# Performance work log

Hardware: AMD Instinct MI355X
Metric: run time of the kernel (lower is better)

## Reference

```python
import jax, jax.numpy as jnp
import numpy as np


def _lyndon_indices(c, d):
    """All Lyndon words of length <= d over alphabet {0..c-1} via Duval's algorithm,
    mapped to flat indices into the flattened signature (levels 1..d concatenated,
    first letter most significant within each level). Static numpy computation."""
    words = []
    w = [-1]
    while w:
        w[-1] += 1
        words.append(tuple(w))
        m = len(w)
        while len(w) < d:
            w.append(w[len(w) - m])
        while w and w[-1] == c - 1:
            w.pop()
    words.sort(key=lambda t: (len(t), t))  # group by word length, lexicographic within
    offsets = np.concatenate([[0], np.cumsum([c ** k for k in range(1, d + 1)])])
    idx = []
    for word in words:
        pos = 0
        for letter in word:
            pos = pos * c + letter
        idx.append(int(offsets[len(word) - 1]) + pos)
    return np.asarray(idx, dtype=np.int64)


def _split_levels(sig, c, d):
    levels, start = [], 0
    for k in range(1, d + 1):
        n = c ** k
        levels.append(sig[:, start:start + n])  # (B, c^k)
        start += n
    return levels


def _mul_by_S(P, S, d):
    """Graded product P (x) S in the truncated tensor algebra (zero scalar parts).
    P[i], S[i] are level-(i+1) components of shape (B, c^(i+1)) or None."""
    B = S[0].shape[0]
    out = [None] * d
    for m in range(d):  # output level m+1
        acc = None
        for i in range(m):  # P level i+1 combines with S level m-i
            if P[i] is None:
                continue
            t = jnp.einsum('bi,bj->bij', P[i], S[m - 1 - i]).reshape(B, -1)
            acc = t if acc is None else acc + t
        out[m] = acc
    return out


def _log_signature_flat(sig, c, d):
    """log(1 + S) truncated at depth d, flattened levels 1..d."""
    S = _split_levels(sig, c, d)
    L = list(S)  # n=1 term (coefficient +1)
    P = S
    for n in range(2, d + 1):
        P = _mul_by_S(P, S, d)  # P = S^{(x) n}, levels < n are None
        coef = ((-1.0) ** (n + 1)) / n
        for k in range(d):
            if P[k] is not None:
                L[k] = L[k] + coef * P[k]
    return jnp.concatenate(L, axis=1)


def setup_inputs() -> dict:
    key = jax.random.key(0)
    channels, depth, batch = 8, 6, 64
    width = sum(channels ** k for k in range(1, depth + 1))  # 299592
    signature = jax.random.normal(key, (batch, width), dtype=jnp.float32) * 0.1
    return {"signature": signature, "channels": channels, "depth": depth}


def reference(signature, channels, depth):
    idx = jnp.asarray(_lyndon_indices(channels, depth))
    log_sig = _log_signature_flat(signature, channels, depth)  # (B, width)
    return log_sig[:, idx]  # Lyndon-word coefficients ('words' mode)
```

## Files before the change

### kernel.cpp

```cpp
#include <hip/hip_runtime.h>

#define NWIDTH 299592
#define NOUT   51360

typedef unsigned long long ull;
typedef unsigned short u16;

__device__ const int g_B2[8] = {8, 15, 21, 26, 30, 33, 35, 36};
__device__ const int g_B3[8] = {36, 92, 134, 164, 184, 196, 202, 204};
__device__ const int g_B4[8] = {204, 624, 897, 1062, 1152, 1194, 1209, 1212};
__device__ const int g_B5[8] = {1212, 4404, 6210, 7140, 7560, 7716, 7758, 7764};
__device__ const int g_C6[8] = {0, 24052, 35861, 41016, 42926, 43480, 43587, 43596};
__device__ const int g_uj1[16] = {0,0,0,0,0,0, 1,1,1,1, 2,2, 3, 4, 5, 6};
__device__ const int g_ur0[16] = {0, 4009, 8018, 12027, 16036, 20044,
                                  24052, 27005, 29957, 32909,
                                  35861, 38439, 41016, 42926, 43480, 43587};
__device__ const int g_ur1[16] = {4009, 8018, 12027, 16036, 20044, 24052,
                                  27005, 29957, 32909, 35861,
                                  38439, 41016, 42926, 43480, 43587, 43596};
__device__ const int g_ualg[16] = {1,0,0,0,0,0, 1,0,0,0, 1,0, 1, 1, 1, 1};

__device__ __forceinline__ bool is_lyndon6(unsigned p) {
  const unsigned mask = (1u << 18) - 1u;
#pragma unroll
  for (int k = 1; k < 6; ++k) {
    unsigned rot = ((p << (3 * k)) & mask) | (p >> (18 - 3 * k));
    if (p >= rot) return false;
  }
  return true;
}
__device__ __forceinline__ bool is_lyndon(unsigned p, int n) {
  const unsigned nb = 3u * (unsigned)n;
  const unsigned mask = (1u << nb) - 1u;
  for (int k = 1; k < n; ++k) {
    unsigned rot = ((p << (3 * k)) & mask) | (p >> (nb - 3 * k));
    if (p >= rot) return false;
  }
  return true;
}

__global__ __launch_bounds__(1024) void lyndon_prep(u16* __restrict__ pos16) {
  __shared__ int wsum[16];
  const int tid = threadIdx.x, lane = tid & 63, wv = tid >> 6;
  const int j = blockIdx.x;
  const unsigned pb = ((unsigned)j << 15) | ((unsigned)tid << 5);
  unsigned lm = 0;
  int c = 0;
  for (int i = 0; i < 32; ++i)
    if (is_lyndon6(pb | (unsigned)i)) { lm |= 1u << i; ++c; }
  int pref = c;
  for (int d = 1; d < 64; d <<= 1) { int t = __shfl_up(pref, d); if (lane >= d) pref += t; }
  if (lane == 63) wsum[wv] = pref;
  __syncthreads();
  int base = 0;
  for (int i = 0; i < wv; ++i) base += wsum[i];
  int ex = g_C6[j] + base + pref - c;
  unsigned m = lm;
  const int p0 = tid << 5;
  while (m) {
    const int bit = __builtin_ctz(m);
    pos16[ex++] = (u16)(p0 + bit);
    m &= m - 1;
  }
}

#define L_S3  0
#define L_S2  512
#define L_S1  576
#define L_PA  584
#define L_PB  1168
#define L_A2  1752
#define L_A3  1760
#define L_A4  1824
#define L_W4  2336
#define L_W5  2344
#define L_A5  2352
#define L_PL  6448
#define L_TOT 8456

__global__ __launch_bounds__(512)
void logsig_fused(const float* __restrict__ sig,
                  const u16* __restrict__ pos16,
                  float* __restrict__ out) {
  __shared__ __align__(16) float sm[L_TOT];
  int* W4i = (int*)(sm + L_W4);
  int* W5i = (int*)(sm + L_W5);
  u16* PL  = (u16*)(sm + L_PL);

  const int tid = threadIdx.x, lane = tid & 63, wv = tid >> 6;
  const int bid = blockIdx.x;
  const int xcd = bid & 7;
  const int rr  = bid >> 3;
  const int b   = xcd * 8 + (rr >> 4);
  const int u   = rr & 15;
  const int j1  = g_uj1[u];
  const bool isalg = g_ualg[u] != 0;
  const int r0 = g_ur0[u], r1 = g_ur1[u];
  const int cnt = r1 - r0;

  const float* __restrict__ S   = sig + (size_t)b * NWIDTH;
  const float* __restrict__ S4g = S + 584;
  const float* __restrict__ S5g = S + 4680;
  const float* __restrict__ S6j = S + 37448 + (size_t)j1 * 32768;
  float* __restrict__ outb = out + (size_t)b * NOUT;

  const float p1 = S[j1];
  const float c2p1 = -0.5f * p1;
  const int q4 = tid << 2;

  sm[L_S3 + tid] = S[72 + tid];
  if (tid < 64) sm[L_S2 + tid] = S[8 + tid];
  if (tid < 8)  sm[L_S1 + tid] = S[tid];
  if (tid < 8)  sm[L_PA + tid]      = S[8 + j1 * 8 + tid];
  if (tid < 64) sm[L_PA + 8 + tid]  = S[72 + j1 * 64 + tid];
  sm[L_PA + 72 + tid] = S4g[j1 * 512 + tid];
  for (int i = tid; i < cnt; i += 512) PL[i] = pos16[r0 + i];
  float p5[8];
  {
    float4 va = *(const float4*)(S5g + j1 * 4096 + q4);
    float4 vb = *(const float4*)(S5g + j1 * 4096 + 2048 + q4);
    p5[0] = va.x; p5[1] = va.y; p5[2] = va.z; p5[3] = va.w;
    p5[4] = vb.x; p5[5] = vb.y; p5[6] = vb.z; p5[7] = vb.w;
  }
  float a5[8] = {0.f, 0.f, 0.f, 0.f, 0.f, 0.f, 0.f, 0.f};
  float a4 = 0.f, a3 = 0.f, a2 = 0.f;

  ull m4 = 0;
  unsigned fm5a = 0, fm5b = 0;
  int exA = 0, exB = 0;
  if (isalg) {
    bool f4 = is_lyndon(((unsigned)j1 << 9) | (unsigned)tid, 4);
    m4 = __ballot(f4);
    if (lane == 0) W4i[wv] = __popcll(m4);
    int c5a = 0, c5b = 0;
#pragma unroll
    for (int e = 0; e < 4; ++e) {
      if (is_lyndon(((unsigned)j1 << 12) | (unsigned)(q4 + e), 5)) { fm5a |= 1u << e; ++c5a; }
      if (is_lyndon(((unsigned)j1 << 12) | (unsigned)(2048 + q4 + e), 5)) { fm5b |= 1u << e; ++c5b; }
    }
    int prefpk = c5a | (c5b << 16);
    for (int d = 1; d < 64; d <<= 1) { int t = __shfl_up(prefpk, d); if (lane >= d) prefpk += t; }
    if (lane == 63) W5i[wv] = prefpk;
    exA = (prefpk & 0xffff) - c5a;
    exB = (prefpk >> 16) - c5b;
  }
  __syncthreads();

  const float s1t = sm[L_S1 + (tid & 7)];
  float s1q4[4];
#pragma unroll
  for (int e = 0; e < 4; ++e) s1q4[e] = sm[L_S1 + ((tid & 1) << 2) + e];

  const float coefs[7] = {0.f, 0.f, -0.5f, 1.f / 3.f, -0.25f, 0.2f, -1.f / 6.f};
#pragma unroll
  for (int n = 2; n <= 5; ++n) {
    const float coef = coefs[n];
    const int RP = (n & 1) ? L_PB : L_PA;
    const int WP = (n & 1) ? L_PA : L_PB;
    a4 += coef * sm[RP + 72 + tid];
    if (tid < 64) a3 += coef * sm[RP + 8 + tid];
    if (tid < 8)  a2 += coef * sm[RP + tid];
    float t4 = sm[RP + 8 + (tid >> 3)] * s1t
             + sm[RP + (tid >> 6)] * sm[L_S2 + (tid & 63)];
    if (n == 2) t4 += p1 * sm[L_S3 + tid];
    float t3 = 0.f, t2 = 0.f;
    if (tid < 64) {
      t3 = sm[RP + (tid >> 3)] * s1t;
      if (n == 2) t3 += p1 * sm[L_S2 + tid];
    }
    if (tid < 8 && n == 2) t2 = p1 * s1t;
    {
      const float rp4a = sm[RP + 72 + (tid >> 1)];
      const float rp4b = sm[RP + 72 + 256 + (tid >> 1)];
      const float rp3a = sm[RP + 8 + (tid >> 4)];
      const float rp3b = sm[RP + 8 + 32 + (tid >> 4)];
      const float rp2a = sm[RP + (tid >> 7)];
      const float rp2b = sm[RP + 4 + (tid >> 7)];
      const float4 s2v = *(const float4*)(sm + L_S2 + (q4 & 63));
      const float4 s3v = *(const float4*)(sm + L_S3 + (q4 & 511));
      const float s2q[4] = {s2v.x, s2v.y, s2v.z, s2v.w};
      const float s3q[4] = {s3v.x, s3v.y, s3v.z, s3v.w};
#pragma unroll
      for (int e = 0; e < 4; ++e) {
        a5[e]     += coef * p5[e];
        a5[4 + e] += coef * p5[4 + e];
        p5[e]     = rp4a * s1q4[e] + rp3a * s2q[e] + rp2a * s3q[e];
        p5[4 + e] = rp4b * s1q4[e] + rp3b * s2q[e] + rp2b * s3q[e];
      }
      if (n == 2) {
        const float4 s4va = *(const float4*)(S4g + q4);
        const float4 s4vb = *(const float4*)(S4g + 2048 + q4);
        const float s4qa[4] = {s4va.x, s4va.y, s4va.z, s4va.w};
        const float s4qb[4] = {s4vb.x, s4vb.y, s4vb.z, s4vb.w};
#pragma unroll
        for (int e = 0; e < 4; ++e) {
          p5[e] += p1 * s4qa[e];
          p5[4 + e] += p1 * s4qb[e];
        }
      }
    }
    sm[WP + 72 + tid] = t4;
    if (tid < 64) sm[WP + 8 + tid] = t3;
    if (tid < 8)  sm[WP + tid]     = t2;
    __syncthreads();
  }
#pragma unroll
  for (int e = 0; e < 8; ++e) a5[e] += coefs[6] * p5[e];

  sm[L_A4 + tid] = a4;
  if (tid < 64) sm[L_A3 + tid] = a3;
  if (tid < 8)  sm[L_A2 + tid] = a2;
  *(float4*)(sm + L_A5 + q4)        = make_float4(a5[0], a5[1], a5[2], a5[3]);
  *(float4*)(sm + L_A5 + 2048 + q4) = make_float4(a5[4], a5[5], a5[6], a5[7]);
  __syncthreads();

  if (isalg) {
    float l2v = 0.f, l3v = 0.f;
    if (tid < 8)
      l2v = sm[L_S2 + j1 * 8 + tid] + c2p1 * s1t;
    if (tid < 64)
      l3v = sm[L_S3 + j1 * 64 + tid] + sm[L_A2 + (tid >> 3)] * s1t
          + c2p1 * sm[L_S2 + tid];
    const float l4v = S4g[j1 * 512 + tid] + sm[L_A3 + (tid >> 3)] * s1t
                    + sm[L_A2 + (tid >> 6)] * sm[L_S2 + (tid & 63)]
                    + c2p1 * sm[L_S3 + tid];
    float l5a[4], l5b[4];
    {
      const float4 via  = *(const float4*)(S5g + j1 * 4096 + q4);
      const float4 vib  = *(const float4*)(S5g + j1 * 4096 + 2048 + q4);
      const float4 s4va = *(const float4*)(S4g + q4);
      const float4 s4vb = *(const float4*)(S4g + 2048 + q4);
      const float4 s2v  = *(const float4*)(sm + L_S2 + (q4 & 63));
      const float4 s3v  = *(const float4*)(sm + L_S3 + (q4 & 511));
      const float l5ia[4] = {via.x, via.y, via.z, via.w};
      const float l5ib[4] = {vib.x, vib.y, vib.z, vib.w};
      const float s4qa[4] = {s4va.x, s4va.y, s4va.z, s4va.w};
      const float s4qb[4] = {s4vb.x, s4vb.y, s4vb.z, s4vb.w};
      const float s2q[4]  = {s2v.x, s2v.y, s2v.z, s2v.w};
      const float s3q[4]  = {s3v.x, s3v.y, s3v.z, s3v.w};
      const float a4a = sm[L_A4 + (tid >> 1)],  a4b = sm[L_A4 + 256 + (tid >> 1)];
      const float a3a = sm[L_A3 + (tid >> 4)],  a3b = sm[L_A3 + 32 + (tid >> 4)];
      const float a2a = sm[L_A2 + (tid >> 7)],  a2b = sm[L_A2 + 4 + (tid >> 7)];
#pragma unroll
      for (int e = 0; e < 4; ++e) {
        l5a[e] = l5ia[e] + a4a * s1q4[e] + a3a * s2q[e] + a2a * s3q[e] + c2p1 * s4qa[e];
        l5b[e] = l5ib[e] + a4b * s1q4[e] + a3b * s2q[e] + a2b * s3q[e] + c2p1 * s4qb[e];
      }
    }
    if (tid == 0) {
      outb[j1] = p1;
      if (j1 == 0) outb[7] = sm[L_S1 + 7];
    }
    if (tid < 8 && tid > j1) outb[g_B2[j1] + tid - j1 - 1] = l2v;
    if (tid < 64) {
      bool f3 = is_lyndon(((unsigned)j1 << 6) | (unsigned)tid, 3);
      ull m3 = __ballot(f3);
      if (f3) outb[g_B3[j1] + __popcll(m3 & ((1ull << lane) - 1ull))] = l3v;
    }
    {
      int base = 0;
      for (int i = 0; i < wv; ++i) base += W4i[i];
      if ((m4 >> lane) & 1ull)
        outb[g_B4[j1] + base + __popcll(m4 & ((1ull << lane) - 1ull))] = l4v;
    }
    {
      int baseA = 0, baseB = 0, totalA = 0;
#pragma unroll
      for (int i = 0; i < 8; ++i) {
        int w = W5i[i];
        totalA += w & 0xffff;
        if (i < wv) { baseA += w & 0xffff; baseB += w >> 16; }
      }
      int slotA = g_B5[j1] + baseA + exA;
      int slotB = g_B5[j1] + totalA + baseB + exB;
#pragma unroll
      for (int e = 0; e < 4; ++e)
        if ((fm5a >> e) & 1u) outb[slotA++] = l5a[e];
#pragma unroll
      for (int e = 0; e < 4; ++e)
        if ((fm5b >> e) & 1u) outb[slotB++] = l5b[e];
    }
  }

  float* __restrict__ outr = outb + 7764 + r0;
  int i = tid;
  for (; i + 512 < cnt; i += 1024) {
    const int pl0 = PL[i];
    const int pl1 = PL[i + 512];
    const float x60 = S6j[pl0], x61 = S6j[pl1];
    const float x50 = S5g[pl0], x51 = S5g[pl1];
    const float x40 = S4g[pl0 & 4095], x41 = S4g[pl1 & 4095];
    float v0 = x60
             + sm[L_A5 + (pl0 >> 3)] * sm[L_S1 + (pl0 & 7)]
             + sm[L_A4 + (pl0 >> 6)] * sm[L_S2 + (pl0 & 63)]
             + sm[L_A3 + (pl0 >> 9)] * sm[L_S3 + (pl0 & 511)]
             + sm[L_A2 + (pl0 >> 12)] * x40
             + c2p1 * x50;
    float v1 = x61
             + sm[L_A5 + (pl1 >> 3)] * sm[L_S1 + (pl1 & 7)]
             + sm[L_A4 + (pl1 >> 6)] * sm[L_S2 + (pl1 & 63)]
             + sm[L_A3 + (pl1 >> 9)] * sm[L_S3 + (pl1 & 511)]
             + sm[L_A2 + (pl1 >> 12)] * x41
             + c2p1 * x51;
    outr[i] = v0;
    outr[i + 512] = v1;
  }
  if (i < cnt) {
    const int pl = PL[i];
    float v = S6j[pl]
            + sm[L_A5 + (pl >> 3)] * sm[L_S1 + (pl & 7)]
            + sm[L_A4 + (pl >> 6)] * sm[L_S2 + (pl & 63)]
            + sm[L_A3 + (pl >> 9)] * sm[L_S3 + (pl & 511)]
            + sm[L_A2 + (pl >> 12)] * S4g[pl & 4095]
            + c2p1 * S5g[pl];
    outr[i] = v;
  }
}


extern "C" void kernel_launch(void* const* d_in, const int* in_sizes, int n_in,
                              void* d_out, int out_size, void* d_ws, size_t ws_size,
                              hipStream_t stream) {
  const float* sig = (const float*)d_in[0];
  float* out = (float*)d_out;
  u16* pos16 = (u16*)d_ws;

  lyndon_prep<<<7, 1024, 0, stream>>>(pos16);
  logsig_fused<<<1024, 512, 0, stream>>>(sig, pos16, out);
}
```

Measured before the change: 43.86 us.

## Replace iterative tensor-power recurrence with closed-form per-level coefficient sums

Replaces the four-iteration loop that built successive tensor powers in shared memory, with a barrier per iteration, by direct closed-form expressions for the level-2..4 prefix coefficients of the level-5 and level-6 terms. Level-5 results are then computed in one pass from the level-5 signature block plus these coefficients, which removes several __syncthreads and the duplicated level-5 recomputation in the output branch. The level-6 loop is also simplified from a two-at-a-time unrolled form to a plain stride loop, which may reduce memory-level parallelism. The new algebra must match the reference recurrence exactly, and that equivalence is hard to check.

```diff
diff --git a/kernel.cpp b/kernel.cpp
--- a/kernel.cpp
+++ b/kernel.cpp
@@ -67,24 +67,25 @@
 #define L_S3  0
 #define L_S2  512
 #define L_S1  576
-#define L_PA  584
-#define L_PB  1168
-#define L_A2  1752
-#define L_A3  1760
-#define L_A4  1824
-#define L_W4  2336
-#define L_W5  2344
-#define L_A5  2352
-#define L_PL  6448
-#define L_TOT 8456
+#define L_A2  584
+#define L_A3  592
+#define L_A4  656
+#define L_W2  1168
+#define L_W3  1176
+#define L_W4  1240
+#define L_W4i 1752
+#define L_W5i 1760
+#define L_A5  1768
+#define L_PL  5864
+#define L_TOT 7872
 
 __global__ __launch_bounds__(512)
 void logsig_fused(const float* __restrict__ sig,
                   const u16* __restrict__ pos16,
                   float* __restrict__ out) {
   __shared__ __align__(16) float sm[L_TOT];
-  int* W4i = (int*)(sm + L_W4);
-  int* W5i = (int*)(sm + L_W5);
+  int* W4i = (int*)(sm + L_W4i);
+  int* W5i = (int*)(sm + L_W5i);
   u16* PL  = (u16*)(sm + L_PL);
 
   const int tid = threadIdx.x, lane = tid & 63, wv = tid >> 6;
@@ -105,16 +106,16 @@
   float* __restrict__ outb = out + (size_t)b * NOUT;
 
   const float p1 = S[j1];
-  const float c2p1 = -0.5f * p1;
+  const float c2 = -0.5f, c3 = 1.f / 3.f, c4 = -0.25f, c5 = 0.2f, c6 = -1.f / 6.f;
+  const float c2p1 = c2 * p1;
+  const float c3p1 = c3 * p1;
   const int q4 = tid << 2;
 
   sm[L_S3 + tid] = S[72 + tid];
   if (tid < 64) sm[L_S2 + tid] = S[8 + tid];
   if (tid < 8)  sm[L_S1 + tid] = S[tid];
-  if (tid < 8)  sm[L_PA + tid]      = S[8 + j1 * 8 + tid];
-  if (tid < 64) sm[L_PA + 8 + tid]  = S[72 + j1 * 64 + tid];
-  sm[L_PA + 72 + tid] = S4g[j1 * 512 + tid];
   for (int i = tid; i < cnt; i += 512) PL[i] = pos16[r0 + i];
+  const float s4p = S4g[j1 * 512 + tid];
   float p5[8];
   {
     float4 va = *(const float4*)(S5g + j1 * 4096 + q4);
@@ -122,8 +123,9 @@
     p5[0] = va.x; p5[1] = va.y; p5[2] = va.z; p5[3] = va.w;
     p5[4] = vb.x; p5[5] = vb.y; p5[6] = vb.z; p5[7] = vb.w;
   }
-  float a5[8] = {0.f, 0.f, 0.f, 0.f, 0.f, 0.f, 0.f, 0.f};
-  float a4 = 0.f, a3 = 0.f, a2 = 0.f;
+  float4 s4qa, s4qb;
+  s4qa = *(const float4*)(S4g + q4);
+  s4qb = *(const float4*)(S4g + 2048 + q4);
 
   ull m4 = 0;
   unsigned fm5a = 0, fm5b = 0;
@@ -146,73 +148,68 @@
   }
   __syncthreads();
 
+  {
+    const int x = tid;
+    const float s1_4 = sm[L_S1 + (x & 7)];
+    const float s1_3 = sm[L_S1 + ((x >> 3) & 7)];
+    const float s1_2 = sm[L_S1 + (x >> 6)];
+    const float s3p  = sm[L_S3 + j1 * 64 + (x >> 3)];
+    const float s2p  = sm[L_S2 + j1 * 8 + (x >> 6)];
+    const float w4_2 = s3p * s1_4 + s2p * sm[L_S2 + (x & 63)] + p1 * sm[L_S3 + x];
+    const float w4_3 = (s2p * s1_3 + p1 * sm[L_S2 + (x >> 3)]) * s1_4
+                     + p1 * s1_2 * sm[L_S2 + (x & 63)];
+    const float w4_4 = p1 * s1_2 * s1_3 * s1_4;
+    sm[L_A4 + x] = c2 * s4p + c3 * w4_2 + c4 * w4_3 + c5 * w4_4;
+    sm[L_W4 + x] = c3 * s4p + c4 * w4_2 + c5 * w4_3 + c6 * w4_4;
+  }
+  if (tid < 64) {
+    const int y = tid;
+    const float w3_2 = sm[L_S2 + j1 * 8 + (y >> 3)] * sm[L_S1 + (y & 7)]
+                     + p1 * sm[L_S2 + y];
+    const float w3_3 = p1 * sm[L_S1 + (y >> 3)] * sm[L_S1 + (y & 7)];
+    const float s3py = sm[L_S3 + j1 * 64 + y];
+    sm[L_A3 + y] = c2 * s3py + c3 * w3_2 + c4 * w3_3;
+    sm[L_W3 + y] = c3 * s3py + c4 * w3_2 + c5 * w3_3;
+  }
+  if (tid < 8) {
+    const int z = tid;
+    const float s2pz = sm[L_S2 + j1 * 8 + z];
+    const float s1z  = sm[L_S1 + z];
+    sm[L_A2 + z] = c2 * s2pz + c3 * p1 * s1z;
+    sm[L_W2 + z] = c3 * s2pz + c4 * p1 * s1z;
+  }
+  __syncthreads();
+
   const float s1t = sm[L_S1 + (tid & 7)];
   float s1q4[4];
 #pragma unroll
   for (int e = 0; e < 4; ++e) s1q4[e] = sm[L_S1 + ((tid & 1) << 2) + e];
 
-  const float coefs[7] = {0.f, 0.f, -0.5f, 1.f / 3.f, -0.25f, 0.2f, -1.f / 6.f};
-#pragma unroll
-  for (int n = 2; n <= 5; ++n) {
-    const float coef = coefs[n];
-    const int RP = (n & 1) ? L_PB : L_PA;
-    const int WP = (n & 1) ? L_PA : L_PB;
-    a4 += coef * sm[RP + 72 + tid];
-    if (tid < 64) a3 += coef * sm[RP + 8 + tid];
-    if (tid < 8)  a2 += coef * sm[RP + tid];
-    float t4 = sm[RP + 8 + (tid >> 3)] * s1t
-             + sm[RP + (tid >> 6)] * sm[L_S2 + (tid & 63)];
-    if (n == 2) t4 += p1 * sm[L_S3 + tid];
-    float t3 = 0.f, t2 = 0.f;
-    if (tid < 64) {
-      t3 = sm[RP + (tid >> 3)] * s1t;
-      if (n == 2) t3 += p1 * sm[L_S2 + tid];
-    }
-    if (tid < 8 && n == 2) t2 = p1 * s1t;
-    {
-      const float rp4a = sm[RP + 72 + (tid >> 1)];
-      const float rp4b = sm[RP + 72 + 256 + (tid >> 1)];
-      const float rp3a = sm[RP + 8 + (tid >> 4)];
-      const float rp3b = sm[RP + 8 + 32 + (tid >> 4)];
-      const float rp2a = sm[RP + (tid >> 7)];
-      const float rp2b = sm[RP + 4 + (tid >> 7)];
-      const float4 s2v = *(const float4*)(sm + L_S2 + (q4 & 63));
-      const float4 s3v = *(const float4*)(sm + L_S3 + (q4 & 511));
-      const float s2q[4] = {s2v.x, s2v.y, s2v.z, s2v.w};
-      const float s3q[4] = {s3v.x, s3v.y, s3v.z, s3v.w};
-#pragma unroll
-      for (int e = 0; e < 4; ++e) {
-        a5[e]     += coef * p5[e];
-        a5[4 + e] += coef * p5[4 + e];
-        p5[e]     = rp4a * s1q4[e] + rp3a * s2q[e] + rp2a * s3q[e];
-        p5[4 + e] = rp4b * s1q4[e] + rp3b * s2q[e] + rp2b * s3q[e];
-      }
-      if (n == 2) {
-        const float4 s4va = *(const float4*)(S4g + q4);
-        const float4 s4vb = *(const float4*)(S4g + 2048 + q4);
-        const float s4qa[4] = {s4va.x, s4va.y, s4va.z, s4va.w};
-        const float s4qb[4] = {s4vb.x, s4vb.y, s4vb.z, s4vb.w};
-#pragma unroll
-        for (int e = 0; e < 4; ++e) {
-          p5[e] += p1 * s4qa[e];
-          p5[4 + e] += p1 * s4qb[e];
-        }
-      }
-    }
-    sm[WP + 72 + tid] = t4;
-    if (tid < 64) sm[WP + 8 + tid] = t3;
-    if (tid < 8)  sm[WP + tid]     = t2;
-    __syncthreads();
-  }
-#pragma unroll
-  for (int e = 0; e < 8; ++e) a5[e] += coefs[6] * p5[e];
-
-  sm[L_A4 + tid] = a4;
-  if (tid < 64) sm[L_A3 + tid] = a3;
-  if (tid < 8)  sm[L_A2 + tid] = a2;
-  *(float4*)(sm + L_A5 + q4)        = make_float4(a5[0], a5[1], a5[2], a5[3]);
-  *(float4*)(sm + L_A5 + 2048 + q4) = make_float4(a5[4], a5[5], a5[6], a5[7]);
-  __syncthreads();
+  float l5a[4], l5b[4];
+  {
+    const float W4a = sm[L_W4 + (tid >> 1)],       W4b = sm[L_W4 + 256 + (tid >> 1)];
+    const float A4a = sm[L_A4 + (tid >> 1)],       A4b = sm[L_A4 + 256 + (tid >> 1)];
+    const float W3a = sm[L_W3 + (tid >> 4)],       W3b = sm[L_W3 + 32 + (tid >> 4)];
+    const float A3a = sm[L_A3 + (tid >> 4)],       A3b = sm[L_A3 + 32 + (tid >> 4)];
+    const float W2a = sm[L_W2 + (tid >> 7)],       W2b = sm[L_W2 + 4 + (tid >> 7)];
+    const float A2a = sm[L_A2 + (tid >> 7)],       A2b = sm[L_A2 + 4 + (tid >> 7)];
+    const float4 s2v = *(const float4*)(sm + L_S2 + (q4 & 63));
+    const float4 s3v = *(const float4*)(sm + L_S3 + (q4 & 511));
+    const float s2q[4] = {s2v.x, s2v.y, s2v.z, s2v.w};
+    const float s3q[4] = {s3v.x, s3v.y, s3v.z, s3v.w};
+    const float s4a[4] = {s4qa.x, s4qa.y, s4qa.z, s4qa.w};
+    const float s4b[4] = {s4qb.x, s4qb.y, s4qb.z, s4qb.w};
+    float a5A[4], a5B[4];
+#pragma unroll
+    for (int e = 0; e < 4; ++e) {
+      a5A[e] = c2 * p5[e]     + W4a * s1q4[e] + W3a * s2q[e] + W2a * s3q[e] + c3p1 * s4a[e];
+      a5B[e] = c2 * p5[4 + e] + W4b * s1q4[e] + W3b * s2q[e] + W2b * s3q[e] + c3p1 * s4b[e];
+      l5a[e] = p5[e]     + A4a * s1q4[e] + A3a * s2q[e] + A2a * s3q[e] + c2p1 * s4a[e];
+      l5b[e] = p5[4 + e] + A4b * s1q4[e] + A3b * s2q[e] + A2b * s3q[e] + c2p1 * s4b[e];
+    }
+    *(float4*)(sm + L_A5 + q4)        = make_float4(a5A[0], a5A[1], a5A[2], a5A[3]);
+    *(float4*)(sm + L_A5 + 2048 + q4) = make_float4(a5B[0], a5B[1], a5B[2], a5B[3]);
+  }
 
   if (isalg) {
     float l2v = 0.f, l3v = 0.f;
@@ -221,32 +218,9 @@
     if (tid < 64)
       l3v = sm[L_S3 + j1 * 64 + tid] + sm[L_A2 + (tid >> 3)] * s1t
           + c2p1 * sm[L_S2 + tid];
-    const float l4v = S4g[j1 * 512 + tid] + sm[L_A3 + (tid >> 3)] * s1t
+    const float l4v = s4p + sm[L_A3 + (tid >> 3)] * s1t
                     + sm[L_A2 + (tid >> 6)] * sm[L_S2 + (tid & 63)]
                     + c2p1 * sm[L_S3 + tid];
-    float l5a[4], l5b[4];
-    {
-      const float4 via  = *(const float4*)(S5g + j1 * 4096 + q4);
-      const float4 vib  = *(const float4*)(S5g + j1 * 4096 + 2048 + q4);
-      const float4 s4va = *(const float4*)(S4g + q4);
-      const float4 s4vb = *(const float4*)(S4g + 2048 + q4);
-      const float4 s2v  = *(const float4*)(sm + L_S2 + (q4 & 63));
-      const float4 s3v  = *(const float4*)(sm + L_S3 + (q4 & 511));
-      const float l5ia[4] = {via.x, via.y, via.z, via.w};
-      const float l5ib[4] = {vib.x, vib.y, vib.z, vib.w};
-      const float s4qa[4] = {s4va.x, s4va.y, s4va.z, s4va.w};
-      const float s4qb[4] = {s4vb.x, s4vb.y, s4vb.z, s4vb.w};
-      const float s2q[4]  = {s2v.x, s2v.y, s2v.z, s2v.w};
-      const float s3q[4]  = {s3v.x, s3v.y, s3v.z, s3v.w};
-      const float a4a = sm[L_A4 + (tid >> 1)],  a4b = sm[L_A4 + 256 + (tid >> 1)];
-      const float a3a = sm[L_A3 + (tid >> 4)],  a3b = sm[L_A3 + 32 + (tid >> 4)];
-      const float a2a = sm[L_A2 + (tid >> 7)],  a2b = sm[L_A2 + 4 + (tid >> 7)];
-#pragma unroll
-      for (int e = 0; e < 4; ++e) {
-        l5a[e] = l5ia[e] + a4a * s1q4[e] + a3a * s2q[e] + a2a * s3q[e] + c2p1 * s4qa[e];
-        l5b[e] = l5ib[e] + a4b * s1q4[e] + a3b * s2q[e] + a2b * s3q[e] + c2p1 * s4qb[e];
-      }
-    }
     if (tid == 0) {
       outb[j1] = p1;
       if (j1 == 0) outb[7] = sm[L_S1 + 7];
@@ -281,31 +255,10 @@
         if ((fm5b >> e) & 1u) outb[slotB++] = l5b[e];
     }
   }
+  __syncthreads();
 
   float* __restrict__ outr = outb + 7764 + r0;
-  int i = tid;
-  for (; i + 512 < cnt; i += 1024) {
-    const int pl0 = PL[i];
-    const int pl1 = PL[i + 512];
-    const float x60 = S6j[pl0], x61 = S6j[pl1];
-    const float x50 = S5g[pl0], x51 = S5g[pl1];
-    const float x40 = S4g[pl0 & 4095], x41 = S4g[pl1 & 4095];
-    float v0 = x60
-             + sm[L_A5 + (pl0 >> 3)] * sm[L_S1 + (pl0 & 7)]
-             + sm[L_A4 + (pl0 >> 6)] * sm[L_S2 + (pl0 & 63)]
-             + sm[L_A3 + (pl0 >> 9)] * sm[L_S3 + (pl0 & 511)]
-             + sm[L_A2 + (pl0 >> 12)] * x40
-             + c2p1 * x50;
-    float v1 = x61
-             + sm[L_A5 + (pl1 >> 3)] * sm[L_S1 + (pl1 & 7)]
-             + sm[L_A4 + (pl1 >> 6)] * sm[L_S2 + (pl1 & 63)]
-             + sm[L_A3 + (pl1 >> 9)] * sm[L_S3 + (pl1 & 511)]
-             + sm[L_A2 + (pl1 >> 12)] * x41
-             + c2p1 * x51;
-    outr[i] = v0;
-    outr[i + 512] = v1;
-  }
-  if (i < cnt) {
+  for (int i = tid; i < cnt; i += 512) {
     const int pl = PL[i];
     float v = S6j[pl]
             + sm[L_A5 + (pl >> 3)] * sm[L_S1 + (pl & 7)]
```

New measurement: 40.29 us (median of 3 runs). 8.1% less time.
